# Optimization experiments

Hardware: AMD Instinct MI355X
Metric: run time of the kernel (lower is better)

The kernel has to match this reference:

```python
import jax, jax.numpy as jnp
import numpy as np

DIM = 256
HEADS = 8
HID = int(DIM * 2.66)  # 680
EPS = 1e-5


def _dwconv3x3(x, k):
    # x: [B,C,H,W], k: [C,1,3,3] depthwise
    return jax.lax.conv_general_dilated(
        x, k, window_strides=(1, 1), padding='SAME',
        feature_group_count=k.shape[0],
        dimension_numbers=('NCHW', 'OIHW', 'NCHW'))


def _conv1x1(x, w):
    # w: [O, C]
    return jnp.einsum('bchw,oc->bohw', x, w)


def _layernorm(x, w, b):
    # WithBias LayerNorm over channel dim (per spatial location), unbiased=False var
    mu = jnp.mean(x, axis=1, keepdims=True)
    var = jnp.var(x, axis=1, keepdims=True)
    return (x - mu) / jnp.sqrt(var + EPS) * w[None, :, None, None] + b[None, :, None, None]


def setup_inputs() -> dict:
    key = jax.random.key(0)
    ks = jax.random.split(key, 8)
    B, C, H, W = 8, DIM, 64, 64
    s = 0.02
    return {
        'x': jax.random.normal(ks[0], (B, C, H, W), jnp.float32),
        'y': jax.random.normal(ks[1], (B, C, H, W), jnp.float32),
        'ln1x_w': jnp.ones((C,), jnp.float32), 'ln1x_b': jnp.zeros((C,), jnp.float32),
        'ln1y_w': jnp.ones((C,), jnp.float32), 'ln1y_b': jnp.zeros((C,), jnp.float32),
        'ln2_w': jnp.ones((C,), jnp.float32), 'ln2_b': jnp.zeros((C,), jnp.float32),
        'temperature': jnp.ones((HEADS, 1, 1), jnp.float32),
        'qkv_dw': jax.random.normal(ks[2], (3 * C, 1, 3, 3), jnp.float32) * s,
        'attn_proj_w': jax.random.normal(ks[3], (C, C), jnp.float32) * s,
        'ffn_in_w': jax.random.normal(ks[4], (2 * HID, C), jnp.float32) * s,
        'ffn_dw': jax.random.normal(ks[5], (2 * HID, 1, 3, 3), jnp.float32) * s,
        'ffn_out_w': jax.random.normal(ks[6], (C, HID), jnp.float32) * s,
    }


def reference(x, y, ln1x_w, ln1x_b, ln1y_w, ln1y_b, ln2_w, ln2_b,
              temperature, qkv_dw, attn_proj_w, ffn_in_w, ffn_dw, ffn_out_w):
    B, C, H, W = x.shape
    ch = C // HEADS
    n = H * W

    # --- Mutual channel attention ---
    xn = _layernorm(x, ln1x_w, ln1x_b)
    yn = _layernorm(y, ln1y_w, ln1y_b)
    qkv = _dwconv3x3(jnp.concatenate((xn, yn, yn), axis=1), qkv_dw)
    q, k, v = jnp.split(qkv, 3, axis=1)
    q = q.reshape(B, HEADS, ch, n)
    k = k.reshape(B, HEADS, ch, n)
    v = v.reshape(B, HEADS, ch, n)
    # L2-normalize along spatial (hw) axis, torch eps=1e-12
    q = q / jnp.maximum(jnp.linalg.norm(q, axis=-1, keepdims=True), 1e-12)
    k = k / jnp.maximum(jnp.linalg.norm(k, axis=-1, keepdims=True), 1e-12)
    attn = jnp.einsum('bhcn,bhdn->bhcd', q, k) * temperature  # [B,H,c,c]
    attn = jax.nn.softmax(attn, axis=-1)
    out = jnp.einsum('bhcd,bhdn->bhcn', attn, v).reshape(B, C, H, W)
    x = x + _conv1x1(out, attn_proj_w)

    # --- Gated dwconv FFN ---
    t = _conv1x1(_layernorm(x, ln2_w, ln2_b), ffn_in_w)
    t = _dwconv3x3(t, ffn_dw)
    t1, t2 = jnp.split(t, 2, axis=1)
    t = jax.nn.gelu(t1, approximate=False) * t2
    x = x + _conv1x1(t, ffn_out_w)
    return x
```

## Files before the change

kernel.cpp:

```cpp
#include <hip/hip_runtime.h>
#include <hip/hip_bf16.h>
#include <math.h>

#define BATCH 8
#define CDIM 256
#define HEADS 8
#define CH 32
#define NSP 4096
#define HID 680
#define QKV_CH 768
#define FFN_CH 1360
#define HIDP 704
#define FFNP 1408
#define GSPLIT 16

typedef _Float16 half8 __attribute__((ext_vector_type(8)));
typedef float floatx4 __attribute__((ext_vector_type(4)));

__device__ inline void gload_lds16(const _Float16* g, _Float16* l) {
  __builtin_amdgcn_global_load_lds(
      (const __attribute__((address_space(1))) unsigned int*)g,
      (__attribute__((address_space(3))) unsigned int*)l, 16, 0, 0);
}

__global__ __launch_bounds__(256) void ln_kernel(
    const float* __restrict__ X, const float* __restrict__ w,
    const float* __restrict__ bia, float* __restrict__ Y) {
  int idx = blockIdx.x * 256 + threadIdx.x;
  int b = idx >> 12;
  int p = idx & 4095;
  const float* xp = X + ((size_t)b * CDIM) * NSP + p;
  float s = 0.f, s2 = 0.f;
  for (int c = 0; c < CDIM; ++c) {
    float v = xp[(size_t)c * NSP];
    s += v; s2 += v * v;
  }
  float mu  = s * (1.f / CDIM);
  float var = s2 * (1.f / CDIM) - mu * mu;
  float inv = 1.0f / sqrtf(var + 1e-5f);
  float* yp = Y + ((size_t)b * CDIM) * NSP + p;
  for (int c = 0; c < CDIM; ++c) {
    float v = xp[(size_t)c * NSP];
    yp[(size_t)c * NSP] = (v - mu) * inv * w[c] + bia[c];
  }
}

__global__ __launch_bounds__(256) void dwconv_qkv_kernel(
    const float* __restrict__ xn, const float* __restrict__ yn,
    const float* __restrict__ kw, float* __restrict__ out) {
  __shared__ float sm[66 * 68];
  int bc = blockIdx.x;
  int b = bc >> 9;
  int c = bc & 511;
  bool isq = (c < 256);
  int ch = isq ? c : c - 256;
  const float* src = (isq ? xn : yn) + ((size_t)(b * CDIM + ch)) * NSP;
  int tid = threadIdx.x;
  for (int i = tid; i < 66 * 68; i += 256) sm[i] = 0.f;
  __syncthreads();
  {
    int r = tid >> 2, xq = (tid & 3) * 16;
    const float* sp = src + r * 64 + xq;
    float4 v0 = ((const float4*)sp)[0];
    float4 v1 = ((const float4*)sp)[1];
    float4 v2 = ((const float4*)sp)[2];
    float4 v3 = ((const float4*)sp)[3];
    float* lp = sm + (r + 1) * 68 + 1 + xq;
    lp[0]=v0.x; lp[1]=v0.y; lp[2]=v0.z;  lp[3]=v0.w;
    lp[4]=v1.x; lp[5]=v1.y; lp[6]=v1.z;  lp[7]=v1.w;
    lp[8]=v2.x; lp[9]=v2.y; lp[10]=v2.z; lp[11]=v2.w;
    lp[12]=v3.x;lp[13]=v3.y;lp[14]=v3.z; lp[15]=v3.w;
  }
  __syncthreads();
  int r = tid >> 2, xs = (tid & 3) * 16;
  float row0[18], row1[18], row2[18];
  {
    const float* q0 = sm + (r + 0) * 68 + xs;
    const float* q1 = sm + (r + 1) * 68 + xs;
    const float* q2 = sm + (r + 2) * 68 + xs;
#pragma unroll
    for (int j = 0; j < 4; ++j) {
      float4 a0 = *(const float4*)(q0 + j * 4);
      float4 a1 = *(const float4*)(q1 + j * 4);
      float4 a2 = *(const float4*)(q2 + j * 4);
      row0[j*4+0]=a0.x; row0[j*4+1]=a0.y; row0[j*4+2]=a0.z; row0[j*4+3]=a0.w;
      row1[j*4+0]=a1.x; row1[j*4+1]=a1.y; row1[j*4+2]=a1.z; row1[j*4+3]=a1.w;
      row2[j*4+0]=a2.x; row2[j*4+1]=a2.y; row2[j*4+2]=a2.z; row2[j*4+3]=a2.w;
    }
    row0[16]=q0[16]; row0[17]=q0[17];
    row1[16]=q1[16]; row1[17]=q1[17];
    row2[16]=q2[16]; row2[17]=q2[17];
  }
  int nouts = isq ? 1 : 2;
  int kcs[2];
  kcs[0] = isq ? c : (256 + ch);
  kcs[1] = 512 + ch;
  for (int oi = 0; oi < nouts; ++oi) {
    int kc = kcs[oi];
    float k9[9];
#pragma unroll
    for (int i = 0; i < 9; ++i) k9[i] = kw[kc * 9 + i];
    float acc[16];
#pragma unroll
    for (int i = 0; i < 16; ++i) {
      acc[i] = row0[i]*k9[0] + row0[i+1]*k9[1] + row0[i+2]*k9[2]
             + row1[i]*k9[3] + row1[i+1]*k9[4] + row1[i+2]*k9[5]
             + row2[i]*k9[6] + row2[i+1]*k9[7] + row2[i+2]*k9[8];
    }
    float* op = out + ((size_t)b * QKV_CH + kc) * NSP + r * 64 + xs;
#pragma unroll
    for (int j = 0; j < 4; ++j)
      ((float4*)op)[j] = make_float4(acc[j*4+0], acc[j*4+1], acc[j*4+2], acc[j*4+3]);
  }
}

__global__ __launch_bounds__(256) void attn_gram_kernel(
    const float* __restrict__ qkv, float* __restrict__ Gp,
    float* __restrict__ Np) {
  __shared__ __align__(16) _Float16 lq[32 * 264];
  __shared__ __align__(16) _Float16 lk[32 * 264];
  int bi = blockIdx.x;
  int split = bi & (GSPLIT - 1);
  int bh = bi / GSPLIT;
  int b = bh >> 3, h = bh & 7;
  int tid = threadIdx.x;
  int row = tid >> 3, cg = (tid & 7) * 32;
  int n0 = split * (NSP / GSPLIT);
  const float* qp = qkv + ((size_t)(b * QKV_CH) + h * CH + row) * NSP + n0 + cg;
  const float* kp = qkv + ((size_t)(b * QKV_CH) + 256 + h * CH + row) * NSP + n0 + cg;
  float sq = 0.f, sk = 0.f;
  _Float16* lqd = lq + row * 264 + cg;
  _Float16* lkd = lk + row * 264 + cg;
#pragma unroll
  for (int j = 0; j < 4; ++j) {
    float4 a0 = *(const float4*)(qp + j * 8);
    float4 a1 = *(const float4*)(qp + j * 8 + 4);
    sq += a0.x*a0.x + a0.y*a0.y + a0.z*a0.z + a0.w*a0.w
        + a1.x*a1.x + a1.y*a1.y + a1.z*a1.z + a1.w*a1.w;
    half8 hv = {(_Float16)a0.x,(_Float16)a0.y,(_Float16)a0.z,(_Float16)a0.w,
                (_Float16)a1.x,(_Float16)a1.y,(_Float16)a1.z,(_Float16)a1.w};
    *(half8*)(lqd + j * 8) = hv;
    float4 b0 = *(const float4*)(kp + j * 8);
    float4 b1 = *(const float4*)(kp + j * 8 + 4);
    sk += b0.x*b0.x + b0.y*b0.y + b0.z*b0.z + b0.w*b0.w
        + b1.x*b1.x + b1.y*b1.y + b1.z*b1.z + b1.w*b1.w;
    half8 hw = {(_Float16)b0.x,(_Float16)b0.y,(_Float16)b0.z,(_Float16)b0.w,
                (_Float16)b1.x,(_Float16)b1.y,(_Float16)b1.z,(_Float16)b1.w};
    *(half8*)(lkd + j * 8) = hw;
  }
  __syncthreads();
  int lane = tid & 63, w = tid >> 6;
  int wr = w >> 1, wc = w & 1;
  int lm = lane & 15, g = lane >> 4;
  floatx4 acc = {0.f, 0.f, 0.f, 0.f};
#pragma unroll
  for (int kk = 0; kk < 8; ++kk) {
    half8 av = *(const half8*)(lq + (wr * 16 + lm) * 264 + kk * 32 + g * 8);
    half8 bv = *(const half8*)(lk + (wc * 16 + lm) * 264 + kk * 32 + g * 8);
    acc = __builtin_amdgcn_mfma_f32_16x16x32_f16(av, bv, acc, 0, 0, 0);
  }
  sq += __shfl_xor(sq, 1); sq += __shfl_xor(sq, 2); sq += __shfl_xor(sq, 4);
  sk += __shfl_xor(sk, 1); sk += __shfl_xor(sk, 2); sk += __shfl_xor(sk, 4);
  if ((tid & 7) == 0) {
    float* np = Np + ((size_t)bh * GSPLIT + split) * 64;
    np[row] = sq;
    np[32 + row] = sk;
  }
  float* gp = Gp + ((size_t)bh * GSPLIT + split) * 1024;
#pragma unroll
  for (int r = 0; r < 4; ++r) {
    int i = wr * 16 + g * 4 + r, j = wc * 16 + lm;
    gp[i * 32 + j] = acc[r];
  }
}

__global__ __launch_bounds__(256) void attn_softmax_kernel(
    const float* __restrict__ Gp, const float* __restrict__ Np,
    const float* __restrict__ temp, float* __restrict__ attn) {
  __shared__ float G[1024];
  __shared__ float qn[32], kn[32];
  int bh = blockIdx.x;
  int tid = threadIdx.x;
  const float* gp = Gp + (size_t)bh * GSPLIT * 1024;
#pragma unroll
  for (int e = tid; e < 1024; e += 256) {
    float s = 0.f;
#pragma unroll
    for (int sp = 0; sp < GSPLIT; ++sp) s += gp[sp * 1024 + e];
    G[e] = s;
  }
  if (tid < 64) {
    const float* np = Np + (size_t)bh * GSPLIT * 64;
    float s = 0.f;
#pragma unroll
    for (int sp = 0; sp < GSPLIT; ++sp) s += np[sp * 64 + tid];
    float nv = fmaxf(sqrtf(s), 1e-12f);
    if (tid < 32) qn[tid] = nv; else kn[tid - 32] = nv;
  }
  __syncthreads();
  if (tid < 32) {
    int c = tid;
    float t = temp[bh & 7];
    float iq = 1.f / qn[c];
    float vals[32];
    float m = -1e30f;
#pragma unroll
    for (int d = 0; d < 32; ++d) {
      float v = G[c * 32 + d] * iq / kn[d] * t;
      vals[d] = v; m = fmaxf(m, v);
    }
    float ss = 0.f;
#pragma unroll
    for (int d = 0; d < 32; ++d) { float e = expf(vals[d] - m); vals[d] = e; ss += e; }
    float inv = 1.f / ss;
#pragma unroll
    for (int d = 0; d < 32; ++d)
      attn[(size_t)bh * 1024 + c * 32 + d] = vals[d] * inv;
  }
}

__global__ __launch_bounds__(256) void av_kernel(
    const float* __restrict__ qkv, const float* __restrict__ attn,
    _Float16* __restrict__ outh) {
  __shared__ float a_s[1024];
  __shared__ float tr[256 * 33];
  int bi = blockIdx.x;
  int chunk = bi & 15;
  int h = (bi >> 4) & 7;
  int b = bi >> 7;
  int tid = threadIdx.x;
  for (int j = tid; j < 1024; j += 256)
    a_s[j] = attn[((size_t)(b * 8 + h)) * 1024 + j];
  __syncthreads();
  int n = chunk * 256 + tid;
  const float* vbase = qkv + ((size_t)(b * QKV_CH + 512 + h * CH)) * NSP + n;
  float acc[32];
#pragma unroll
  for (int c = 0; c < 32; ++c) acc[c] = 0.f;
#pragma unroll 4
  for (int d = 0; d < 32; ++d) {
    float vv = vbase[(size_t)d * NSP];
#pragma unroll
    for (int c = 0; c < 32; ++c) acc[c] += a_s[c * 32 + d] * vv;
  }
#pragma unroll
  for (int c = 0; c < 32; ++c) tr[tid * 33 + c] = acc[c];
  __syncthreads();
#pragma unroll
  for (int it = 0; it < 4; ++it) {
    int gi = it * 256 + tid;
    int row = gi >> 2, gc = gi & 3;
    half8 hv;
#pragma unroll
    for (int e = 0; e < 8; ++e) hv[e] = (_Float16)tr[row * 33 + gc * 8 + e];
    *(half8*)(outh + ((size_t)(b * NSP + chunk * 256 + row)) * CDIM + h * CH + gc * 8) = hv;
  }
}

__global__ __launch_bounds__(256) void convw_kernel(
    const float* __restrict__ src, _Float16* __restrict__ dst,
    int R, int Cs, int Cd, int total) {
  int idx = blockIdx.x * 256 + threadIdx.x;
  if (idx >= total) return;
  int r = idx / Cd, c = idx - r * Cd;
  float v = (r < R && c < Cs) ? src[r * Cs + c] : 0.f;
  dst[idx] = (_Float16)v;
}

__global__ __launch_bounds__(256) void transw_kernel(
    const float* __restrict__ kw, _Float16* __restrict__ wt) {
  int idx = blockIdx.x * 256 + threadIdx.x;
  if (idx >= 2 * 9 * 680) return;
  int h = idx / 6120;
  int rem = idx - h * 6120;
  int ki = rem / 680;
  int c  = rem - ki * 680;
  wt[idx] = (_Float16)kw[(h * 680 + c) * 9 + ki];
}

__global__ __launch_bounds__(256) void ln2_kernel(
    const float* __restrict__ X, float* __restrict__ P,
    const float* __restrict__ w2, const float* __restrict__ b2,
    _Float16* __restrict__ x2nh) {
  __shared__ __align__(16) _Float16 lw[4][64 * 72];
  int tid = threadIdx.x;
  int lane = tid & 63, w = tid >> 6;
  int loc = blockIdx.x * 256 + w * 64 + lane;
  int b = loc >> 12, p = loc & 4095;
  const float* xp = X + ((size_t)b * CDIM) * NSP + p;
  float* pp = P + ((size_t)b * CDIM) * NSP + p;
  float s = 0.f, s2 = 0.f;
  for (int c = 0; c < CDIM; ++c) {
    float v = xp[(size_t)c * NSP] + pp[(size_t)c * NSP];
    s += v; s2 += v * v;
  }
  float mu = s * (1.f / CDIM);
  float var = s2 * (1.f / CDIM) - mu * mu;
  float inv = 1.0f / sqrtf(var + 1e-5f);
  _Float16* lwp = lw[w];
  int locb = blockIdx.x * 256 + w * 64;
  for (int cc0 = 0; cc0 < CDIM; cc0 += 64) {
    for (int c = cc0; c < cc0 + 64; ++c) {
      float v = xp[(size_t)c * NSP] + pp[(size_t)c * NSP];
      pp[(size_t)c * NSP] = v;
      lwp[lane * 72 + (c - cc0)] = (_Float16)((v - mu) * inv * w2[c] + b2[c]);
    }
#pragma unroll
    for (int it = 0; it < 8; ++it) {
      int m = it * 64 + lane;
      int row = m >> 3, cg = m & 7;
      half8 hv = *(const half8*)(lwp + row * 72 + cg * 8);
      *(half8*)(x2nh + ((size_t)(locb + row)) * CDIM + cc0 + cg * 8) = hv;
    }
  }
}

template <bool RES, typename OutT>
__global__ __launch_bounds__(256) void gemm_f16_kernel(
    const _Float16* __restrict__ A, size_t sA,
    const _Float16* __restrict__ B, size_t sB,
    const float* __restrict__ R, size_t sR,
    OutT* __restrict__ Y, size_t sY,
    int K, int ldy, int Nj, int gx, int gy) {
  __shared__ __align__(16) _Float16 As[128 * 32];
  __shared__ __align__(16) _Float16 Bs[128 * 32];
  int cpx = gx * gy;
  int sb = (blockIdx.x & 7) * cpx + (blockIdx.x >> 3);
  int bx = sb % gx;
  int tmp = sb / gx;
  int by = tmp % gy;
  int bz = tmp / gy;
  int tid = threadIdx.x;
  int lane = tid & 63;
  int w = tid >> 6;
  int wr = w >> 1, wc = w & 1;
  int lm = lane & 15, g = lane >> 4;
  int i0 = by * 128;
  int j0 = bx * 128;
  const _Float16* Ab = A + (size_t)bz * sA;
  const _Float16* Bb = B + (size_t)bz * sB;

  floatx4 acc[4][4];
#pragma unroll
  for (int mi = 0; mi < 4; ++mi)
#pragma unroll
    for (int ni = 0; ni < 4; ++ni) acc[mi][ni] = {0.f, 0.f, 0.f, 0.f};

  for (int k0 = 0; k0 < K; k0 += 32) {
#pragma unroll
    for (int jj = 0; jj < 2; ++jj) {
      int idx = jj * 256 + tid;
      int row = idx >> 2, gc = idx & 3;
      int base = idx & ~63;
      gload_lds16(Ab + (size_t)(i0 + row) * K + k0 + gc * 8, As + base * 8);
      gload_lds16(Bb + (size_t)(j0 + row) * K + k0 + gc * 8, Bs + base * 8);
    }
    __syncthreads();
    half8 ha[4], hb[4];
#pragma unroll
    for (int mi = 0; mi < 4; ++mi)
      ha[mi] = *(const half8*)(As + (wr * 64 + mi * 16 + lm) * 32 + g * 8);
#pragma unroll
    for (int ni = 0; ni < 4; ++ni)
      hb[ni] = *(const half8*)(Bs + (wc * 64 + ni * 16 + lm) * 32 + g * 8);
#pragma unroll
    for (int mi = 0; mi < 4; ++mi)
#pragma unroll
      for (int ni = 0; ni < 4; ++ni)
        acc[mi][ni] = __builtin_amdgcn_mfma_f32_16x16x32_f16(
            ha[mi], hb[ni], acc[mi][ni], 0, 0, 0);
    __syncthreads();
  }

  const float* Rb = RES ? (R + (size_t)bz * sR) : nullptr;
  OutT* Yb = Y + (size_t)bz * sY;
#pragma unroll
  for (int mi = 0; mi < 4; ++mi) {
#pragma unroll
    for (int ni = 0; ni < 4; ++ni) {
      int j = j0 + wc * 64 + ni * 16 + lm;
      if (j >= Nj) continue;
#pragma unroll
      for (int r = 0; r < 4; ++r) {
        int i = i0 + wr * 64 + mi * 16 + g * 4 + r;
        size_t o = (size_t)i * ldy + j;
        float v = acc[mi][ni][r];
        if (RES) v += Rb[o];
        Yb[o] = (OutT)v;
      }
    }
  }
}

#define DWG_NBLK (BATCH * NSP * 88 / 256)
__global__ __launch_bounds__(256) void dwgate_kernel(
    const _Float16* __restrict__ t, const _Float16* __restrict__ wt,
    _Float16* __restrict__ g) {
  int sb = (blockIdx.x & 7) * (DWG_NBLK / 8) + (blockIdx.x >> 3);
  int idx = sb * 256 + threadIdx.x;
  int grp = idx % 88;
  int bp  = idx / 88;
  int c0 = grp * 8;
  _Float16* gp = g + (size_t)bp * HIDP + c0;
  if (grp >= 85) {
    half8 z = {};
    *(half8*)gp = z;
    return;
  }
  int p = bp & 4095;
  int y0 = p >> 6, x0 = p & 63;
  const _Float16* tb = t + (size_t)bp * FFN_CH;
  half8 accA = {}, accB = {};
#pragma unroll
  for (int dy = -1; dy <= 1; ++dy) {
    int yy = y0 + dy;
    if ((unsigned)yy > 63u) continue;
#pragma unroll
    for (int dx = -1; dx <= 1; ++dx) {
      int xx = x0 + dx;
      if ((unsigned)xx > 63u) continue;
      int ki = (dy + 1) * 3 + (dx + 1);
      const _Float16* tp = tb + (ptrdiff_t)(dy * 64 + dx) * FFN_CH;
      half8 va = *(const half8*)(tp + c0);
      half8 vb = *(const half8*)(tp + HID + c0);
      half8 wa = *(const half8*)(wt + ki * 680 + c0);
      half8 wb = *(const half8*)(wt + 6120 + ki * 680 + c0);
      accA += va * wa;
      accB += vb * wb;
    }
  }
  half8 r;
#pragma unroll
  for (int e = 0; e < 8; ++e) {
    float a = (float)accA[e];
    float ge = 0.5f * a * (1.f + erff(a * 0.70710678118654752440f));
    r[e] = (_Float16)(ge * (float)accB[e]);
  }
  *(half8*)gp = r;
}

extern "C" void kernel_launch(void* const* d_in, const int* in_sizes, int n_in,
                              void* d_out, int out_size, void* d_ws, size_t ws_size,
                              hipStream_t stream) {
  const float* x         = (const float*)d_in[0];
  const float* y         = (const float*)d_in[1];
  const float* ln1x_w    = (const float*)d_in[2];
  const float* ln1x_b    = (const float*)d_in[3];
  const float* ln1y_w    = (const float*)d_in[4];
  const float* ln1y_b    = (const float*)d_in[5];
  const float* ln2_w     = (const float*)d_in[6];
  const float* ln2_b     = (const float*)d_in[7];
  const float* temperature = (const float*)d_in[8];
  const float* qkv_dw    = (const float*)d_in[9];
  const float* attn_proj_w = (const float*)d_in[10];
  const float* ffn_in_w  = (const float*)d_in[11];
  const float* ffn_dw    = (const float*)d_in[12];
  const float* ffn_out_w = (const float*)d_in[13];
  float* out = (float*)d_out;
  char* wsb = (char*)d_ws;

  const size_t SZ_CN4 = (size_t)BATCH * CDIM * NSP * 4;
  const size_t off_A   = 0;
  const size_t off_B   = SZ_CN4;
  const size_t off_C   = 2 * SZ_CN4;
  const size_t off_D   = off_C + (size_t)BATCH * QKV_CH * NSP * 4;
  const size_t off_gp  = off_D + 20u * 1024 * 1024;
  const size_t off_np  = off_gp + (size_t)64 * GSPLIT * 1024 * 4;
  const size_t off_sm  = off_D + (size_t)BATCH * NSP * HIDP * 2;
  const size_t off_attn = off_sm;
  const size_t off_wp   = off_attn + 262144;
  const size_t off_wf   = off_wp + (size_t)CDIM * CDIM * 2;
  const size_t off_wo   = off_wf + (size_t)FFNP * CDIM * 2;
  const size_t off_wt   = off_wo + (size_t)CDIM * HIDP * 2;

  float*    xn    = (float*)(wsb + off_A);
  float*    yn    = (float*)(wsb + off_B);
  float*    qkv   = (float*)(wsb + off_C);
  _Float16* tbuf  = (_Float16*)(wsb + off_C);
  _Float16* av_h  = (_Float16*)(wsb + off_D);
  _Float16* g_h   = (_Float16*)(wsb + off_D);
  float*    Gp    = (float*)(wsb + off_gp);
  float*    Np    = (float*)(wsb + off_np);
  float*    P     = (float*)(wsb + off_A);
  _Float16* x2n_h = (_Float16*)(wsb + off_B);
  float*    attn  = (float*)(wsb + off_attn);
  _Float16* wp_h  = (_Float16*)(wsb + off_wp);
  _Float16* wf_h  = (_Float16*)(wsb + off_wf);
  _Float16* wo_h  = (_Float16*)(wsb + off_wo);
  _Float16* wt_h  = (_Float16*)(wsb + off_wt);

  convw_kernel<<<(CDIM * CDIM + 255) / 256, 256, 0, stream>>>(
      attn_proj_w, wp_h, CDIM, CDIM, CDIM, CDIM * CDIM);
  convw_kernel<<<(FFNP * CDIM + 255) / 256, 256, 0, stream>>>(
      ffn_in_w, wf_h, FFN_CH, CDIM, CDIM, FFNP * CDIM);
  convw_kernel<<<(CDIM * HIDP + 255) / 256, 256, 0, stream>>>(
      ffn_out_w, wo_h, CDIM, HID, HIDP, CDIM * HIDP);
  transw_kernel<<<48, 256, 0, stream>>>(ffn_dw, wt_h);

  ln_kernel<<<BATCH * NSP / 256, 256, 0, stream>>>(x, ln1x_w, ln1x_b, xn);
  ln_kernel<<<BATCH * NSP / 256, 256, 0, stream>>>(y, ln1y_w, ln1y_b, yn);
  dwconv_qkv_kernel<<<BATCH * 512, 256, 0, stream>>>(xn, yn, qkv_dw, qkv);
  attn_gram_kernel<<<BATCH * HEADS * GSPLIT, 256, 0, stream>>>(qkv, Gp, Np);
  attn_softmax_kernel<<<BATCH * HEADS, 256, 0, stream>>>(Gp, Np, temperature, attn);
  av_kernel<<<BATCH * HEADS * (NSP / 256), 256, 0, stream>>>(qkv, attn, av_h);

  gemm_f16_kernel<false, float><<<32 * 2 * BATCH, 256, 0, stream>>>(
      wp_h, (size_t)0, av_h, (size_t)NSP * CDIM, nullptr, (size_t)0,
      P, (size_t)CDIM * NSP, CDIM, NSP, NSP, 32, 2);

  ln2_kernel<<<BATCH * NSP / 256, 256, 0, stream>>>(x, P, ln2_w, ln2_b, x2n_h);

  gemm_f16_kernel<false, _Float16><<<11 * 32 * BATCH, 256, 0, stream>>>(
      x2n_h, (size_t)NSP * CDIM, wf_h, (size_t)0, nullptr, (size_t)0,
      tbuf, (size_t)NSP * FFN_CH, CDIM, FFN_CH, FFN_CH, 11, 32);

  dwgate_kernel<<<DWG_NBLK, 256, 0, stream>>>(tbuf, wt_h, g_h);

  gemm_f16_kernel<true, float><<<32 * 2 * BATCH, 256, 0, stream>>>(
      wo_h, (size_t)0, g_h, (size_t)NSP * HIDP, P, (size_t)CDIM * NSP,
      out, (size_t)CDIM * NSP, HIDP, NSP, NSP, 32, 2);
}
```

Measured before the change: 467.6 us.

## Fuse LayerNorm into qkv dwconv, store qkv in fp16, reuse rows in dwgate

The first LayerNorm now only computes per-pixel mean and inverse std for x and y in a single launch. The normalization is applied while loading tiles inside the qkv depthwise conv, so the normalized fp32 tensors are never written or read back. The qkv tensor is stored in fp16, which halves traffic for the Gram and AV kernels, at the cost of some precision in the norms. The FFN dwconv-gate kernel now walks 16 rows per thread with a rolling 3-row register window and keeps the weights in registers, cutting redundant neighbour loads at the price of fewer threads.

```diff
diff --git a/kernel.cpp b/kernel.cpp
--- a/kernel.cpp
+++ b/kernel.cpp
@@ -23,53 +23,61 @@
       (__attribute__((address_space(3))) unsigned int*)l, 16, 0, 0);
 }
 
-__global__ __launch_bounds__(256) void ln_kernel(
-    const float* __restrict__ X, const float* __restrict__ w,
-    const float* __restrict__ bia, float* __restrict__ Y) {
+__global__ __launch_bounds__(256) void lnstat_kernel(
+    const float* __restrict__ X, const float* __restrict__ Yv,
+    float* __restrict__ muv, float* __restrict__ invv) {
   int idx = blockIdx.x * 256 + threadIdx.x;
-  int b = idx >> 12;
-  int p = idx & 4095;
-  const float* xp = X + ((size_t)b * CDIM) * NSP + p;
+  int which = idx >> 15;
+  int bp = idx & 32767;
+  int b = bp >> 12, p = bp & 4095;
+  const float* src = (which ? Yv : X) + ((size_t)b * CDIM) * NSP + p;
   float s = 0.f, s2 = 0.f;
   for (int c = 0; c < CDIM; ++c) {
-    float v = xp[(size_t)c * NSP];
+    float v = src[(size_t)c * NSP];
     s += v; s2 += v * v;
   }
   float mu  = s * (1.f / CDIM);
   float var = s2 * (1.f / CDIM) - mu * mu;
-  float inv = 1.0f / sqrtf(var + 1e-5f);
-  float* yp = Y + ((size_t)b * CDIM) * NSP + p;
-  for (int c = 0; c < CDIM; ++c) {
-    float v = xp[(size_t)c * NSP];
-    yp[(size_t)c * NSP] = (v - mu) * inv * w[c] + bia[c];
-  }
+  muv[idx]  = mu;
+  invv[idx] = 1.0f / sqrtf(var + 1e-5f);
 }
 
 __global__ __launch_bounds__(256) void dwconv_qkv_kernel(
-    const float* __restrict__ xn, const float* __restrict__ yn,
-    const float* __restrict__ kw, float* __restrict__ out) {
+    const float* __restrict__ X, const float* __restrict__ Yv,
+    const float* __restrict__ w1x, const float* __restrict__ b1x,
+    const float* __restrict__ w1y, const float* __restrict__ b1y,
+    const float* __restrict__ muv, const float* __restrict__ invv,
+    const float* __restrict__ kw, _Float16* __restrict__ out) {
   __shared__ float sm[66 * 68];
   int bc = blockIdx.x;
   int b = bc >> 9;
   int c = bc & 511;
   bool isq = (c < 256);
   int ch = isq ? c : c - 256;
-  const float* src = (isq ? xn : yn) + ((size_t)(b * CDIM + ch)) * NSP;
+  const float* src = (isq ? X : Yv) + ((size_t)(b * CDIM + ch)) * NSP;
+  const float* mup = muv  + (isq ? 0 : 32768) + b * 4096;
+  const float* ivp = invv + (isq ? 0 : 32768) + b * 4096;
+  float wc  = (isq ? w1x : w1y)[ch];
+  float bcv = (isq ? b1x : b1y)[ch];
   int tid = threadIdx.x;
   for (int i = tid; i < 66 * 68; i += 256) sm[i] = 0.f;
   __syncthreads();
   {
     int r = tid >> 2, xq = (tid & 3) * 16;
     const float* sp = src + r * 64 + xq;
-    float4 v0 = ((const float4*)sp)[0];
-    float4 v1 = ((const float4*)sp)[1];
-    float4 v2 = ((const float4*)sp)[2];
-    float4 v3 = ((const float4*)sp)[3];
+    const float* mp = mup + r * 64 + xq;
+    const float* ip = ivp + r * 64 + xq;
     float* lp = sm + (r + 1) * 68 + 1 + xq;
-    lp[0]=v0.x; lp[1]=v0.y; lp[2]=v0.z;  lp[3]=v0.w;
-    lp[4]=v1.x; lp[5]=v1.y; lp[6]=v1.z;  lp[7]=v1.w;
-    lp[8]=v2.x; lp[9]=v2.y; lp[10]=v2.z; lp[11]=v2.w;
-    lp[12]=v3.x;lp[13]=v3.y;lp[14]=v3.z; lp[15]=v3.w;
+#pragma unroll
+    for (int j = 0; j < 4; ++j) {
+      float4 v  = ((const float4*)sp)[j];
+      float4 m  = ((const float4*)mp)[j];
+      float4 iv = ((const float4*)ip)[j];
+      lp[j*4+0] = (v.x - m.x) * iv.x * wc + bcv;
+      lp[j*4+1] = (v.y - m.y) * iv.y * wc + bcv;
+      lp[j*4+2] = (v.z - m.z) * iv.z * wc + bcv;
+      lp[j*4+3] = (v.w - m.w) * iv.w * wc + bcv;
+    }
   }
   __syncthreads();
   int r = tid >> 2, xs = (tid & 3) * 16;
@@ -107,15 +115,17 @@
              + row1[i]*k9[3] + row1[i+1]*k9[4] + row1[i+2]*k9[5]
              + row2[i]*k9[6] + row2[i+1]*k9[7] + row2[i+2]*k9[8];
     }
-    float* op = out + ((size_t)b * QKV_CH + kc) * NSP + r * 64 + xs;
-#pragma unroll
-    for (int j = 0; j < 4; ++j)
-      ((float4*)op)[j] = make_float4(acc[j*4+0], acc[j*4+1], acc[j*4+2], acc[j*4+3]);
+    _Float16* op = out + ((size_t)b * QKV_CH + kc) * NSP + r * 64 + xs;
+    half8 h0, h1;
+#pragma unroll
+    for (int e = 0; e < 8; ++e) { h0[e] = (_Float16)acc[e]; h1[e] = (_Float16)acc[8+e]; }
+    ((half8*)op)[0] = h0;
+    ((half8*)op)[1] = h1;
   }
 }
 
 __global__ __launch_bounds__(256) void attn_gram_kernel(
-    const float* __restrict__ qkv, float* __restrict__ Gp,
+    const _Float16* __restrict__ qkv, float* __restrict__ Gp,
     float* __restrict__ Np) {
   __shared__ __align__(16) _Float16 lq[32 * 264];
   __shared__ __align__(16) _Float16 lk[32 * 264];
@@ -126,26 +136,21 @@
   int tid = threadIdx.x;
   int row = tid >> 3, cg = (tid & 7) * 32;
   int n0 = split * (NSP / GSPLIT);
-  const float* qp = qkv + ((size_t)(b * QKV_CH) + h * CH + row) * NSP + n0 + cg;
-  const float* kp = qkv + ((size_t)(b * QKV_CH) + 256 + h * CH + row) * NSP + n0 + cg;
+  const _Float16* qp = qkv + ((size_t)(b * QKV_CH) + h * CH + row) * NSP + n0 + cg;
+  const _Float16* kp = qkv + ((size_t)(b * QKV_CH) + 256 + h * CH + row) * NSP + n0 + cg;
   float sq = 0.f, sk = 0.f;
   _Float16* lqd = lq + row * 264 + cg;
   _Float16* lkd = lk + row * 264 + cg;
 #pragma unroll
   for (int j = 0; j < 4; ++j) {
-    float4 a0 = *(const float4*)(qp + j * 8);
-    float4 a1 = *(const float4*)(qp + j * 8 + 4);
-    sq += a0.x*a0.x + a0.y*a0.y + a0.z*a0.z + a0.w*a0.w
-        + a1.x*a1.x + a1.y*a1.y + a1.z*a1.z + a1.w*a1.w;
-    half8 hv = {(_Float16)a0.x,(_Float16)a0.y,(_Float16)a0.z,(_Float16)a0.w,
-                (_Float16)a1.x,(_Float16)a1.y,(_Float16)a1.z,(_Float16)a1.w};
+    half8 hv = *(const half8*)(qp + j * 8);
+    half8 hw = *(const half8*)(kp + j * 8);
+#pragma unroll
+    for (int e = 0; e < 8; ++e) {
+      float fq = (float)hv[e]; sq += fq * fq;
+      float fk = (float)hw[e]; sk += fk * fk;
+    }
     *(half8*)(lqd + j * 8) = hv;
-    float4 b0 = *(const float4*)(kp + j * 8);
-    float4 b1 = *(const float4*)(kp + j * 8 + 4);
-    sk += b0.x*b0.x + b0.y*b0.y + b0.z*b0.z + b0.w*b0.w
-        + b1.x*b1.x + b1.y*b1.y + b1.z*b1.z + b1.w*b1.w;
-    half8 hw = {(_Float16)b0.x,(_Float16)b0.y,(_Float16)b0.z,(_Float16)b0.w,
-                (_Float16)b1.x,(_Float16)b1.y,(_Float16)b1.z,(_Float16)b1.w};
     *(half8*)(lkd + j * 8) = hw;
   }
   __syncthreads();
@@ -220,7 +225,7 @@
 }
 
 __global__ __launch_bounds__(256) void av_kernel(
-    const float* __restrict__ qkv, const float* __restrict__ attn,
+    const _Float16* __restrict__ qkv, const float* __restrict__ attn,
     _Float16* __restrict__ outh) {
   __shared__ float a_s[1024];
   __shared__ float tr[256 * 33];
@@ -233,13 +238,13 @@
     a_s[j] = attn[((size_t)(b * 8 + h)) * 1024 + j];
   __syncthreads();
   int n = chunk * 256 + tid;
-  const float* vbase = qkv + ((size_t)(b * QKV_CH + 512 + h * CH)) * NSP + n;
+  const _Float16* vbase = qkv + ((size_t)(b * QKV_CH + 512 + h * CH)) * NSP + n;
   float acc[32];
 #pragma unroll
   for (int c = 0; c < 32; ++c) acc[c] = 0.f;
 #pragma unroll 4
   for (int d = 0; d < 32; ++d) {
-    float vv = vbase[(size_t)d * NSP];
+    float vv = (float)vbase[(size_t)d * NSP];
 #pragma unroll
     for (int c = 0; c < 32; ++c) acc[c] += a_s[c * 32 + d] * vv;
   }
@@ -392,51 +397,79 @@
   }
 }
 
-#define DWG_NBLK (BATCH * NSP * 88 / 256)
+#define DWG_NBLK (BATCH * 64 * 4 * 88 / 256)
 __global__ __launch_bounds__(256) void dwgate_kernel(
     const _Float16* __restrict__ t, const _Float16* __restrict__ wt,
     _Float16* __restrict__ g) {
-  int sb = (blockIdx.x & 7) * (DWG_NBLK / 8) + (blockIdx.x >> 3);
-  int idx = sb * 256 + threadIdx.x;
-  int grp = idx % 88;
-  int bp  = idx / 88;
-  int c0 = grp * 8;
-  _Float16* gp = g + (size_t)bp * HIDP + c0;
-  if (grp >= 85) {
+  int idx = blockIdx.x * 256 + threadIdx.x;
+  int cg = idx % 88;
+  int rest = idx / 88;
+  int ys = rest & 3;
+  int x0 = (rest >> 2) & 63;
+  int b  = rest >> 8;
+  int c0 = cg * 8;
+  int ybeg = ys * 16;
+  size_t gbase = ((size_t)(b * 4096 + ybeg * 64 + x0)) * HIDP + c0;
+  if (cg >= 85) {
     half8 z = {};
-    *(half8*)gp = z;
+#pragma unroll
+    for (int yi = 0; yi < 16; ++yi)
+      *(half8*)(g + gbase + (size_t)yi * 64 * HIDP) = z;
     return;
   }
-  int p = bp & 4095;
-  int y0 = p >> 6, x0 = p & 63;
-  const _Float16* tb = t + (size_t)bp * FFN_CH;
-  half8 accA = {}, accB = {};
-#pragma unroll
-  for (int dy = -1; dy <= 1; ++dy) {
-    int yy = y0 + dy;
-    if ((unsigned)yy > 63u) continue;
-#pragma unroll
-    for (int dx = -1; dx <= 1; ++dx) {
-      int xx = x0 + dx;
-      if ((unsigned)xx > 63u) continue;
-      int ki = (dy + 1) * 3 + (dx + 1);
-      const _Float16* tp = tb + (ptrdiff_t)(dy * 64 + dx) * FFN_CH;
-      half8 va = *(const half8*)(tp + c0);
-      half8 vb = *(const half8*)(tp + HID + c0);
-      half8 wa = *(const half8*)(wt + ki * 680 + c0);
-      half8 wb = *(const half8*)(wt + 6120 + ki * 680 + c0);
-      accA += va * wa;
-      accB += vb * wb;
-    }
-  }
-  half8 r;
-#pragma unroll
-  for (int e = 0; e < 8; ++e) {
-    float a = (float)accA[e];
-    float ge = 0.5f * a * (1.f + erff(a * 0.70710678118654752440f));
-    r[e] = (_Float16)(ge * (float)accB[e]);
-  }
-  *(half8*)gp = r;
+  half8 wa[9], wb[9];
+#pragma unroll
+  for (int k = 0; k < 9; ++k) {
+    wa[k] = *(const half8*)(wt + k * 680 + c0);
+    wb[k] = *(const half8*)(wt + 6120 + k * 680 + c0);
+  }
+  const _Float16* tb = t + ((size_t)b * 4096) * FFN_CH + c0;
+  auto LDA = [&](int yy, int xx) -> half8 {
+    half8 z = {};
+    if ((unsigned)yy > 63u || (unsigned)xx > 63u) return z;
+    return *(const half8*)(tb + ((size_t)(yy * 64 + xx)) * FFN_CH);
+  };
+  auto LDB = [&](int yy, int xx) -> half8 {
+    half8 z = {};
+    if ((unsigned)yy > 63u || (unsigned)xx > 63u) return z;
+    return *(const half8*)(tb + ((size_t)(yy * 64 + xx)) * FFN_CH + HID);
+  };
+  half8 rA[3][3], rB[3][3];
+#pragma unroll
+  for (int dx = 0; dx < 3; ++dx) {
+    rA[0][dx] = LDA(ybeg - 1, x0 + dx - 1); rB[0][dx] = LDB(ybeg - 1, x0 + dx - 1);
+    rA[1][dx] = LDA(ybeg,     x0 + dx - 1); rB[1][dx] = LDB(ybeg,     x0 + dx - 1);
+  }
+#pragma unroll
+  for (int yi = 0; yi < 16; ++yi) {
+    int yn = ybeg + yi + 1;
+#pragma unroll
+    for (int dx = 0; dx < 3; ++dx) {
+      rA[2][dx] = LDA(yn, x0 + dx - 1);
+      rB[2][dx] = LDB(yn, x0 + dx - 1);
+    }
+    half8 accA = {}, accB = {};
+#pragma unroll
+    for (int r = 0; r < 3; ++r)
+#pragma unroll
+      for (int dx = 0; dx < 3; ++dx) {
+        accA += rA[r][dx] * wa[r * 3 + dx];
+        accB += rB[r][dx] * wb[r * 3 + dx];
+      }
+    half8 res;
+#pragma unroll
+    for (int e = 0; e < 8; ++e) {
+      float a = (float)accA[e];
+      float ge = 0.5f * a * (1.f + erff(a * 0.70710678118654752440f));
+      res[e] = (_Float16)(ge * (float)accB[e]);
+    }
+    *(half8*)(g + gbase + (size_t)yi * 64 * HIDP) = res;
+#pragma unroll
+    for (int dx = 0; dx < 3; ++dx) {
+      rA[0][dx] = rA[1][dx]; rA[1][dx] = rA[2][dx];
+      rB[0][dx] = rB[1][dx]; rB[1][dx] = rB[2][dx];
+    }
+  }
 }
 
 extern "C" void kernel_launch(void* const* d_in, const int* in_sizes, int n_in,
@@ -472,10 +505,10 @@
   const size_t off_wf   = off_wp + (size_t)CDIM * CDIM * 2;
   const size_t off_wo   = off_wf + (size_t)FFNP * CDIM * 2;
   const size_t off_wt   = off_wo + (size_t)CDIM * HIDP * 2;
-
-  float*    xn    = (float*)(wsb + off_A);
-  float*    yn    = (float*)(wsb + off_B);
-  float*    qkv   = (float*)(wsb + off_C);
+  const size_t off_mu   = off_wt + 32768;
+  const size_t off_iv   = off_mu + 262144;
+
+  _Float16* qkv   = (_Float16*)(wsb + off_C);
   _Float16* tbuf  = (_Float16*)(wsb + off_C);
   _Float16* av_h  = (_Float16*)(wsb + off_D);
   _Float16* g_h   = (_Float16*)(wsb + off_D);
@@ -488,6 +521,8 @@
   _Float16* wf_h  = (_Float16*)(wsb + off_wf);
   _Float16* wo_h  = (_Float16*)(wsb + off_wo);
   _Float16* wt_h  = (_Float16*)(wsb + off_wt);
+  float*    muv   = (float*)(wsb + off_mu);
+  float*    invv  = (float*)(wsb + off_iv);
 
   convw_kernel<<<(CDIM * CDIM + 255) / 256, 256, 0, stream>>>(
       attn_proj_w, wp_h, CDIM, CDIM, CDIM, CDIM * CDIM);
@@ -497,9 +532,9 @@
       ffn_out_w, wo_h, CDIM, HID, HIDP, CDIM * HIDP);
   transw_kernel<<<48, 256, 0, stream>>>(ffn_dw, wt_h);
 
-  ln_kernel<<<BATCH * NSP / 256, 256, 0, stream>>>(x, ln1x_w, ln1x_b, xn);
-  ln_kernel<<<BATCH * NSP / 256, 256, 0, stream>>>(y, ln1y_w, ln1y_b, yn);
-  dwconv_qkv_kernel<<<BATCH * 512, 256, 0, stream>>>(xn, yn, qkv_dw, qkv);
+  lnstat_kernel<<<256, 256, 0, stream>>>(x, y, muv, invv);
+  dwconv_qkv_kernel<<<BATCH * 512, 256, 0, stream>>>(
+      x, y, ln1x_w, ln1x_b, ln1y_w, ln1y_b, muv, invv, qkv_dw, qkv);
   attn_gram_kernel<<<BATCH * HEADS * GSPLIT, 256, 0, stream>>>(qkv, Gp, Np);
   attn_softmax_kernel<<<BATCH * HEADS, 256, 0, stream>>>(Gp, Np, temperature, attn);
   av_kernel<<<BATCH * HEADS * (NSP / 256), 256, 0, stream>>>(qkv, attn, av_h);
```

Measured after the change: 419.1 us. 10.4% less time.
